# Kernel optimization log

Hardware: AMD Instinct MI355X
Metric: run time of the kernel (lower is better)

Reference implementation:

```python
import jax, jax.numpy as jnp
import numpy as np

TOPK = 2

def setup_inputs() -> dict:
    key = jax.random.key(0)
    ks = jax.random.split(key, 5)
    B, S, D, H, E = 2, 4096, 1024, 2048, 8
    x = jax.random.normal(ks[0], (B, S, D), dtype=jnp.float32)
    router_w = jax.random.normal(ks[1], (E, D), dtype=jnp.float32) * 0.02
    w1 = jax.random.normal(ks[2], (E, D, H), dtype=jnp.float32) * 0.02
    w3 = jax.random.normal(ks[3], (E, D, H), dtype=jnp.float32) * 0.02
    w2 = jax.random.normal(ks[4], (E, H, D), dtype=jnp.float32) * 0.02
    return {"x": x, "router_w": router_w, "w1": w1, "w3": w3, "w2": w2}

def reference(x, router_w, w1, w3, w2):
    B, S, D = x.shape
    E = router_w.shape[0]
    xf = x.reshape(-1, D)                      # [T, D]
    T = xf.shape[0]
    logits = (xf @ router_w.T).astype(jnp.float32)      # [T, E]
    weights, indices = jax.lax.top_k(logits, TOPK)      # [T, k]
    weights = jax.nn.softmax(weights, axis=-1).astype(x.dtype)
    prob = jax.nn.softmax(logits, axis=-1)              # [T, E] fp32
    P = prob.mean(axis=0).astype(x.dtype)               # [E]
    mask = jnp.zeros((T, E), jnp.float32).at[jnp.arange(T)[:, None], indices].set(1.0)
    f = mask.mean(axis=0).astype(x.dtype)               # [E]
    aux_loss = E * jnp.sum(f * P)
    out = jnp.zeros_like(xf)
    for e in range(E):
        # combine weight for expert e per token (0 if not routed here)
        coef = jnp.sum(jnp.where(indices == e, weights, jnp.zeros_like(weights)), axis=-1)  # [T]
        h = jax.nn.silu(xf @ w1[e]) * (xf @ w3[e])      # [T, H] SwiGLU
        out = out + coef[:, None] * (h @ w2[e])         # masked combine == gather/scatter
    return out.reshape(B, S, D), aux_loss
```

## Files before the change

kernel.cpp:

```cpp
#include <hip/hip_runtime.h>
#include <hip/hip_bf16.h>

#define TT 8192
#define DD 1024
#define HH 2048
#define EE 8

typedef __bf16 bf16x8 __attribute__((ext_vector_type(8)));
typedef float floatx4 __attribute__((ext_vector_type(4)));
typedef short shortx8 __attribute__((ext_vector_type(8)));

__device__ __forceinline__ short f2bf(float f) {
  unsigned u = __float_as_uint(f);
  u += 0x7fffu + ((u >> 16) & 1u);
  return (short)(u >> 16);
}

__device__ __forceinline__ float bf2f(short s) {
  return __uint_as_float(((unsigned)(unsigned short)s) << 16);
}

__device__ __forceinline__ void gld16(const void* g, void* l) {
  __builtin_amdgcn_global_load_lds((const __attribute__((address_space(1))) void*)g,
                                   (__attribute__((address_space(3))) void*)l, 16, 0, 0);
}

__global__ __launch_bounds__(256) void router_kernel(
    const float* __restrict__ x, const float* __restrict__ rw,
    int* __restrict__ cpad, float* __restrict__ ppad,
    int* __restrict__ list_token, float* __restrict__ list_coef,
    int* __restrict__ tokpk, float* __restrict__ tokcf,
    short* __restrict__ xb)
{
  __shared__ int   sE0[32], sE1[32], lcnt[EE], sbase[EE], lp0[32], lp1[32];
  __shared__ float sG0[32], sG1[32], sP[EE];
  const int tid = threadIdx.x;
  if (tid < EE) { sP[tid] = 0.f; lcnt[tid] = 0; }
  __syncthreads();
  const int lane = tid & 63, wv = tid >> 6;
  const int t0 = blockIdx.x * 32;
  for (int ti = 0; ti < 8; ++ti) {
    const int s = wv * 8 + ti;
    const int t = t0 + s;
    float sc[EE];
#pragma unroll
    for (int e = 0; e < EE; ++e) sc[e] = 0.f;
#pragma unroll
    for (int j = 0; j < 4; ++j) {
      float4 xv = *(const float4*)(x + (size_t)t * DD + j * 256 + lane * 4);
#pragma unroll
      for (int e = 0; e < EE; ++e) {
        float4 rv = *(const float4*)(rw + e * DD + j * 256 + lane * 4);
        sc[e] += xv.x * rv.x + xv.y * rv.y + xv.z * rv.z + xv.w * rv.w;
      }
      if (xb) {
        short4 sv = make_short4(f2bf(xv.x), f2bf(xv.y), f2bf(xv.z), f2bf(xv.w));
        *(short4*)(xb + (size_t)t * DD + j * 256 + lane * 4) = sv;
      }
    }
#pragma unroll
    for (int off = 32; off > 0; off >>= 1)
#pragma unroll
      for (int e = 0; e < EE; ++e)
        sc[e] += __shfl_down(sc[e], off);
    if (lane == 0) {
      int i0 = 0; float l0 = sc[0];
      for (int e = 1; e < EE; ++e) if (sc[e] > l0) { l0 = sc[e]; i0 = e; }
      int i1 = -1; float l1 = -3.4e38f;
      for (int e = 0; e < EE; ++e) if (e != i0 && sc[e] > l1) { l1 = sc[e]; i1 = e; }
      const float g0 = 1.f / (1.f + __expf(l1 - l0));
      float pr[EE]; float sum = 0.f;
      for (int e = 0; e < EE; ++e) { pr[e] = __expf(sc[e] - l0); sum += pr[e]; }
      const float inv = 1.f / sum;
      for (int e = 0; e < EE; ++e) atomicAdd(&sP[e], pr[e] * inv);
      sE0[s] = i0; sE1[s] = i1; sG0[s] = g0; sG1[s] = 1.f - g0;
    }
  }
  __syncthreads();
  if (tid < 32) {
    lp0[tid] = atomicAdd(&lcnt[sE0[tid]], 1);
    lp1[tid] = atomicAdd(&lcnt[sE1[tid]], 1);
  }
  __syncthreads();
  if (tid < EE) {
    sbase[tid] = atomicAdd(&cpad[tid * 16], lcnt[tid]);
    atomicAdd(&ppad[tid * 16], sP[tid]);
  }
  __syncthreads();
  if (tid < 32) {
    int e0 = sE0[tid], e1 = sE1[tid], t = t0 + tid;
    int p0 = sbase[e0] + lp0[tid];
    int p1 = sbase[e1] + lp1[tid];
    list_token[e0 * TT + p0] = t; list_coef[e0 * TT + p0] = sG0[tid];
    list_token[e1 * TT + p1] = t; list_coef[e1 * TT + p1] = sG1[tid];
    tokpk[t * 2]     = (e0 << 13) | p0;  tokcf[t * 2]     = sG0[tid];
    tokpk[t * 2 + 1] = (e1 << 13) | p1;  tokcf[t * 2 + 1] = sG1[tid];
  }
}

__global__ void aux_kernel(const int* __restrict__ cpad, const float* __restrict__ ppad,
                           int* __restrict__ offsets, float* __restrict__ out_aux)
{
  if (threadIdx.x == 0) {
    float aux = 0.f; int off = 0;
    for (int e = 0; e < EE; ++e) {
      aux += ((float)cpad[e * 16] / (float)TT) * (ppad[e * 16] / (float)TT);
      offsets[e] = off; off += cpad[e * 16];
    }
    *out_aux = aux * (float)EE;
  }
}

__global__ __launch_bounds__(256) void convt13_kernel(const float* __restrict__ w1,
                                                      const float* __restrict__ w3,
                                                      short* __restrict__ out)
{
  __shared__ short T[64 * 74];
  const int t = threadIdx.x;
  const int z = blockIdx.z;
  const int is3 = (z >= EE) ? 1 : 0;
  const int e = is3 ? (z - EE) : z;
  const float* in = (is3 ? w3 : w1) + (size_t)e * DD * HH;
  short* o = out + (size_t)e * DD * HH * 2;
  const int c0 = blockIdx.x * 64, r0 = blockIdx.y * 64;
#pragma unroll
  for (int p = 0; p < 4; ++p) {
    int r = p * 16 + (t >> 4), c4 = (t & 15) * 4;
    float4 v = *(const float4*)(in + (size_t)(r0 + r) * HH + c0 + c4);
    short4 s = make_short4(f2bf(v.x), f2bf(v.y), f2bf(v.z), f2bf(v.w));
    *(short4*)&T[r * 74 + c4] = s;
  }
  __syncthreads();
#pragma unroll
  for (int q = 0; q < 2; ++q) {
    int u = q * 256 + t;
    int oc = u >> 3, k8 = (u & 7) * 8;
    shortx8 s;
#pragma unroll
    for (int j = 0; j < 8; ++j) s[j] = T[(k8 + j) * 74 + oc];
    int c = c0 + oc;
    int grow = 2 * (c & ~31) + (c & 31) + (is3 ? 32 : 0);
    *(shortx8*)&o[(size_t)grow * DD + r0 + k8] = s;
  }
}

__global__ __launch_bounds__(256) void convt_kernel(const float* __restrict__ in, short* __restrict__ out,
                                                    int R, int C)
{
  __shared__ short T[64 * 74];
  const int t = threadIdx.x;
  in  += (size_t)blockIdx.z * R * C;
  out += (size_t)blockIdx.z * R * C;
  const int c0 = blockIdx.x * 64, r0 = blockIdx.y * 64;
#pragma unroll
  for (int p = 0; p < 4; ++p) {
    int r = p * 16 + (t >> 4), c4 = (t & 15) * 4;
    float4 v = *(const float4*)(in + (size_t)(r0 + r) * C + c0 + c4);
    short4 s = make_short4(f2bf(v.x), f2bf(v.y), f2bf(v.z), f2bf(v.w));
    *(short4*)&T[r * 74 + c4] = s;
  }
  __syncthreads();
#pragma unroll
  for (int q = 0; q < 2; ++q) {
    int u = q * 256 + t;
    int oc = u >> 3, k8 = (u & 7) * 8;
    shortx8 s;
#pragma unroll
    for (int j = 0; j < 8; ++j) s[j] = T[(k8 + j) * 74 + oc];
    *(shortx8*)&out[(size_t)(c0 + oc) * R + r0 + k8] = s;
  }
}


#define PH_BAR()  { __builtin_amdgcn_s_barrier(); __builtin_amdgcn_sched_barrier(0); }
#define WAITL0()  { asm volatile("s_waitcnt lgkmcnt(0)" ::: "memory"); __builtin_amdgcn_sched_barrier(0); }
#define WAITVN(n) { asm volatile("s_waitcnt vmcnt(" #n ")" ::: "memory"); __builtin_amdgcn_sched_barrier(0); }

template<int NT>
__device__ __forceinline__ void mma_core(char* SM, int tid,
    const char* a00, const char* a01, const char* a10, const char* a11,
    const char* b00, const char* b01, const char* b10, const char* b11,
    floatx4 (&acc)[8][4])
{
  const int lane = tid & 63, w = tid >> 6;
  const int l16 = lane & 15, quad = lane >> 4;
  const int wm = (w >> 2) & 1, wn = w & 3;
  const int cx = (((l16 >> 1) & 1) << 4) | (((l16 >> 2) & 1) << 5) | ((l16 & 1) << 6);
  const int ck0 = (quad * 16) ^ cx;
  const int arb = (wm * 128 + l16) * 128;
  const int brb = 32768 + (wn * 64 + l16) * 128;
  const int wq = w * 2048;

#define SA_(u,h,p0,p1) { gld16((p0) + (size_t)(u) * 128, SM + (((u) & 1) << 16) + (h) * 16384 + wq); \
                         gld16((p1) + (size_t)(u) * 128, SM + (((u) & 1) << 16) + (h) * 16384 + wq + 1024); }
#define SB_(u,h,p0,p1) { gld16((p0) + (size_t)(u) * 128, SM + (((u) & 1) << 16) + 32768 + (h) * 16384 + wq); \
                         gld16((p1) + (size_t)(u) * 128, SM + (((u) & 1) << 16) + 32768 + (h) * 16384 + wq + 1024); }
#define LA_(mi) { a[mi][0] = *(const bf16x8*)(SM + cur + arb + (mi) * 2048 + ck0); \
                  a[mi][1] = *(const bf16x8*)(SM + cur + arb + (mi) * 2048 + (ck0 ^ 64)); }
#define LB_(ni) { b[ni][0] = *(const bf16x8*)(SM + cur + brb + (ni) * 2048 + ck0); \
                  b[ni][1] = *(const bf16x8*)(SM + cur + brb + (ni) * 2048 + (ck0 ^ 64)); }
#define MM_(mi,ni) { acc[mi][ni] = __builtin_amdgcn_mfma_f32_16x16x32_bf16(a[mi][0], b[ni][0], acc[mi][ni], 0, 0, 0); \
                     acc[mi][ni] = __builtin_amdgcn_mfma_f32_16x16x32_bf16(a[mi][1], b[ni][1], acc[mi][ni], 0, 0, 0); }

  SA_(0, 0, a00, a01); SA_(0, 1, a10, a11);
  SB_(0, 0, b00, b01); SB_(0, 1, b10, b11);
  SA_(1, 0, a00, a01); SA_(1, 1, a10, a11);
  WAITVN(4);
  __builtin_amdgcn_s_barrier();
  __builtin_amdgcn_sched_barrier(0);

#pragma unroll 2
  for (int t = 0; t < NT; ++t) {
    const int cur = (t & 1) << 16;
    bf16x8 a[8][2], b[4][2];
    LA_(0) LA_(1) LA_(2) LA_(3) LB_(0) LB_(1)
    if (t + 1 < NT) SB_(t + 1, 0, b00, b01);
    PH_BAR(); WAITL0();
    __builtin_amdgcn_s_setprio(1);
    MM_(0,0) MM_(1,0) MM_(2,0) MM_(3,0) MM_(0,1) MM_(1,1) MM_(2,1) MM_(3,1)
    __builtin_amdgcn_s_setprio(0);
    PH_BAR();
    LA_(4) LA_(5) LA_(6) LA_(7) LB_(2) LB_(3)
    if (t + 1 < NT) SB_(t + 1, 1, b10, b11);
    PH_BAR(); WAITL0();
    __builtin_amdgcn_s_setprio(1);
    MM_(4,2) MM_(5,2) MM_(6,2) MM_(7,2) MM_(4,3) MM_(5,3) MM_(6,3) MM_(7,3)
    __builtin_amdgcn_s_setprio(0);
    PH_BAR();
    if (t + 2 < NT) SA_(t + 2, 0, a00, a01);
    PH_BAR();
    __builtin_amdgcn_s_setprio(1);
    MM_(0,2) MM_(1,2) MM_(2,2) MM_(3,2) MM_(0,3) MM_(1,3) MM_(2,3) MM_(3,3)
    __builtin_amdgcn_s_setprio(0);
    PH_BAR();
    if (t + 2 < NT) SA_(t + 2, 1, a10, a11);
    PH_BAR();
    __builtin_amdgcn_s_setprio(1);
    MM_(4,0) MM_(5,0) MM_(6,0) MM_(7,0) MM_(4,1) MM_(5,1) MM_(6,1) MM_(7,1)
    __builtin_amdgcn_s_setprio(0);
    if (t + 2 < NT) { WAITVN(4); } else { WAITVN(0); }
    PH_BAR();
  }
#undef SA_
#undef SB_
#undef LA_
#undef LB_
#undef MM_
}

__global__ __launch_bounds__(512, 2) void g1p_kernel(
    const short* __restrict__ xb, const short* __restrict__ w13t,
    const int* __restrict__ cpad, const int* __restrict__ offsets,
    const int* __restrict__ list_token, short* __restrict__ Hbuf)
{
  const int lin = blockIdx.x + 16 * (blockIdx.y + 32 * blockIdx.z);
  const int xcd = lin & 7, c = lin >> 3;
  const int e = c >> 6, rb = (c >> 1) & 31, nb = (xcd << 1) | (c & 1);
  const int cnt = cpad[e * 16];
  if (rb * 256 >= cnt) return;
  __shared__ char SM[131072];
  const int tid = threadIdx.x;
  const int lane = tid & 63, w = tid >> 6;
  const int srow = lane >> 3;
  const int scol = (((lane ^ (lane >> 4)) & 1) << 4)
                 | ((((lane >> 1) ^ (lane >> 5)) & 1) << 5)
                 | ((((lane >> 2) ^ (lane >> 3)) & 1) << 6);
  const int* lt = list_token + e * TT;
  const char* ap[2][2];
#pragma unroll
  for (int h = 0; h < 2; ++h)
#pragma unroll
    for (int i = 0; i < 2; ++i) {
      int gr = rb * 256 + h * 128 + (w * 2 + i) * 8 + srow;
      int tok = (gr < cnt) ? lt[gr] : lt[0];
      ap[h][i] = (const char*)xb + (size_t)tok * 2048 + scol;
    }
  const char* bb = (const char*)w13t + ((size_t)e * 4096 + nb * 256) * 2048
                 + (size_t)(w * 16 + srow) * 2048 + scol;
  floatx4 acc[8][4] = {};
  mma_core<16>(SM, tid, ap[0][0], ap[0][1], ap[1][0], ap[1][1],
               bb, bb + 8 * 2048, bb + 128 * 2048, bb + 136 * 2048, acc);
  const int off = offsets[e];
  const int l16 = lane & 15, quad = lane >> 4;
  const int wm = (w >> 2) & 1, wn = w & 3;
#pragma unroll
  for (int mi = 0; mi < 8; ++mi)
#pragma unroll
    for (int r = 0; r < 4; ++r) {
      int grow = rb * 256 + wm * 128 + mi * 16 + quad * 4 + r;
      if (grow < cnt) {
        size_t rowbase = (size_t)(off + grow) * HH + nb * 128 + wn * 32;
#pragma unroll
        for (int ni = 0; ni < 2; ++ni) {
          float aa = acc[mi][ni][r], bbv = acc[mi][ni + 2][r];
          float hv = aa / (1.f + __expf(-aa)) * bbv;
          Hbuf[rowbase + ni * 16 + l16] = f2bf(hv);
        }
      }
    }
}

__global__ __launch_bounds__(256, 2) void g2o_kernel(
    const short* __restrict__ Hbuf, const short* __restrict__ w2t,
    const int* __restrict__ cpad, const int* __restrict__ offsets,
    short* __restrict__ Obuf)
{
  const int lin = blockIdx.x + 8 * (blockIdx.y + 64 * blockIdx.z);
  const int xcd = lin & 7, c = lin >> 3;
  const int nb = xcd, e = c >> 6, rb = c & 63;
  const int cnt = cpad[e * 16];
  if (rb * 128 >= cnt) return;
  __shared__ short Asm[128 * 32];
  __shared__ short Bsm[128 * 32];
  const int tid = threadIdx.x, lane = tid & 63, wv = tid >> 6;
  const int wm = (wv >> 1) * 64, wn = (wv & 1) * 64;
  const int quad = lane >> 4, l16 = lane & 15;
  floatx4 acc[4][4] = {{{0.f}}};
  const int off = offsets[e];
  const int qrow = wv * 32 + (lane >> 2);
  const int qcb = (lane & 3) * 16;
  const char* ag = (const char*)(Hbuf + (size_t)(off + rb * 128 + qrow) * HH) + qcb;
  const char* bg = (const char*)(w2t + (size_t)e * DD * HH + (size_t)(nb * 128 + qrow) * HH) + qcb;
  char* al = (char*)Asm + wv * 2048;
  char* bl = (char*)Bsm + wv * 2048;
  int aro[4], bro[4];
#pragma unroll
  for (int mi = 0; mi < 4; ++mi) aro[mi] = (wm + mi * 16 + l16) * 32 + quad * 8;
#pragma unroll
  for (int ni = 0; ni < 4; ++ni) bro[ni] = (wn + ni * 16 + l16) * 32 + quad * 8;

  for (int k0 = 0; k0 < HH; k0 += 32) {
    __syncthreads();
    gld16(ag + (size_t)k0 * 2, al);
    gld16(ag + (size_t)k0 * 2 + 16 * HH * 2, al + 1024);
    gld16(bg + (size_t)k0 * 2, bl);
    gld16(bg + (size_t)k0 * 2 + 16 * HH * 2, bl + 1024);
    __syncthreads();
    bf16x8 af[4], bf[4];
#pragma unroll
    for (int mi = 0; mi < 4; ++mi) af[mi] = *(const bf16x8*)&Asm[aro[mi]];
#pragma unroll
    for (int ni = 0; ni < 4; ++ni) bf[ni] = *(const bf16x8*)&Bsm[bro[ni]];
#pragma unroll
    for (int mi = 0; mi < 4; ++mi)
#pragma unroll
      for (int ni = 0; ni < 4; ++ni)
        acc[mi][ni] = __builtin_amdgcn_mfma_f32_16x16x32_bf16(af[mi], bf[ni], acc[mi][ni], 0, 0, 0);
  }
#pragma unroll
  for (int mi = 0; mi < 4; ++mi)
#pragma unroll
    for (int r = 0; r < 4; ++r) {
      int row = wm + mi * 16 + quad * 4 + r;
      int grow = rb * 128 + row;
      if (grow < cnt) {
        short* orow = Obuf + (size_t)(off + grow) * DD + nb * 128 + wn;
#pragma unroll
        for (int ni = 0; ni < 4; ++ni)
          orow[ni * 16 + l16] = f2bf(acc[mi][ni][r]);
      }
    }
}

__global__ __launch_bounds__(256) void combine_kernel(
    const short* __restrict__ Obuf, const int* __restrict__ offsets,
    const int* __restrict__ tokpk, const float* __restrict__ tokcf,
    float* __restrict__ out)
{
  const int tid = threadIdx.x, lane = tid & 63, wv = tid >> 6;
  const int t = blockIdx.x * 4 + wv;
  const int pk0 = tokpk[t * 2], pk1 = tokpk[t * 2 + 1];
  const float c0 = tokcf[t * 2], c1 = tokcf[t * 2 + 1];
  const size_t r0 = (size_t)(offsets[pk0 >> 13] + (pk0 & 8191)) * DD;
  const size_t r1 = (size_t)(offsets[pk1 >> 13] + (pk1 & 8191)) * DD;
  float* orow = out + (size_t)t * DD;
#pragma unroll
  for (int p = 0; p < 2; ++p) {
    int cidx = p * 512 + lane * 8;
    shortx8 a = *(const shortx8*)(Obuf + r0 + cidx);
    shortx8 b = *(const shortx8*)(Obuf + r1 + cidx);
    float v[8];
#pragma unroll
    for (int j = 0; j < 8; ++j) v[j] = c0 * bf2f(a[j]) + c1 * bf2f(b[j]);
    *(float4*)(orow + cidx)     = make_float4(v[0], v[1], v[2], v[3]);
    *(float4*)(orow + cidx + 4) = make_float4(v[4], v[5], v[6], v[7]);
  }
}

__global__ __launch_bounds__(256, 2) void g1s_kernel(
    const float* __restrict__ x, const float* __restrict__ w1, const float* __restrict__ w3,
    const int* __restrict__ cpad, const int* __restrict__ offsets,
    const int* __restrict__ list_token, short* __restrict__ Hbuf)
{
  const int e = blockIdx.z, rb = blockIdx.y, nb = blockIdx.x;
  const int cnt = cpad[e * 16];
  if (rb * 128 >= cnt) return;
  __shared__ short Asm[128 * 40];
  __shared__ short B1sm[128 * 40];
  __shared__ short B3sm[128 * 40];
  const int tid = threadIdx.x, lane = tid & 63, wv = tid >> 6;
  const int wm = (wv >> 1) * 64, wn = (wv & 1) * 64;
  const int quad = lane >> 4, l16 = lane & 15;
  floatx4 acc1[4][4] = {{{0.f}}};
  floatx4 acc3[4][4] = {{{0.f}}};
  const int ar = tid >> 3, ak = (tid & 7) * 4;
  const int bp = tid & 63, bq = tid >> 6;
  const int bswz = (bq ^ ((bp >> 2) & 3)) * 8;
  const int bo0 = (2 * bp) * 40 + bswz, bo1 = bo0 + 40;
  int aro[4], bro[4];
#pragma unroll
  for (int mi = 0; mi < 4; ++mi) aro[mi] = (wm + mi * 16 + l16) * 40 + quad * 8;
#pragma unroll
  for (int ni = 0; ni < 4; ++ni) {
    int nl = wn + ni * 16 + l16;
    bro[ni] = nl * 40 + ((quad ^ ((nl >> 3) & 3)) * 8);
  }
  int tok[4];
#pragma unroll
  for (int i = 0; i < 4; ++i) {
    int gr = rb * 128 + ar + 32 * i;
    tok[i] = (gr < cnt) ? list_token[e * TT + gr] : list_token[e * TT];
  }
  const float* w1e = w1 + (size_t)e * DD * HH + (size_t)nb * 128;
  const float* w3e = w3 + (size_t)e * DD * HH + (size_t)nb * 128;
  for (int k0 = 0; k0 < DD; k0 += 32) {
    __syncthreads();
#pragma unroll
    for (int i = 0; i < 4; ++i) {
      int r = ar + 32 * i;
      float4 v = *(const float4*)(x + (size_t)tok[i] * DD + k0 + ak);
      short4 sv = make_short4(f2bf(v.x), f2bf(v.y), f2bf(v.z), f2bf(v.w));
      *(short4*)&Asm[r * 40 + ak] = sv;
    }
    {
      float2 u[8];
#pragma unroll
      for (int j = 0; j < 8; ++j) u[j] = *(const float2*)(w1e + (size_t)(k0 + bq * 8 + j) * HH + 2 * bp);
      shortx8 p0, p1;
#pragma unroll
      for (int j = 0; j < 8; ++j) { p0[j] = f2bf(u[j].x); p1[j] = f2bf(u[j].y); }
      *(shortx8*)&B1sm[bo0] = p0; *(shortx8*)&B1sm[bo1] = p1;
    }
    {
      float2 u[8];
#pragma unroll
      for (int j = 0; j < 8; ++j) u[j] = *(const float2*)(w3e + (size_t)(k0 + bq * 8 + j) * HH + 2 * bp);
      shortx8 p0, p1;
#pragma unroll
      for (int j = 0; j < 8; ++j) { p0[j] = f2bf(u[j].x); p1[j] = f2bf(u[j].y); }
      *(shortx8*)&B3sm[bo0] = p0; *(shortx8*)&B3sm[bo1] = p1;
    }
    __syncthreads();
    bf16x8 af[4], b1f[4], b3f[4];
#pragma unroll
    for (int mi = 0; mi < 4; ++mi) af[mi] = *(const bf16x8*)&Asm[aro[mi]];
#pragma unroll
    for (int ni = 0; ni < 4; ++ni) {
      b1f[ni] = *(const bf16x8*)&B1sm[bro[ni]];
      b3f[ni] = *(const bf16x8*)&B3sm[bro[ni]];
    }
#pragma unroll
    for (int mi = 0; mi < 4; ++mi)
#pragma unroll
      for (int ni = 0; ni < 4; ++ni) {
        acc1[mi][ni] = __builtin_amdgcn_mfma_f32_16x16x32_bf16(af[mi], b1f[ni], acc1[mi][ni], 0, 0, 0);
        acc3[mi][ni] = __builtin_amdgcn_mfma_f32_16x16x32_bf16(af[mi], b3f[ni], acc3[mi][ni], 0, 0, 0);
      }
  }
  const int off = offsets[e];
#pragma unroll
  for (int mi = 0; mi < 4; ++mi)
#pragma unroll
    for (int r = 0; r < 4; ++r) {
      int row = wm + mi * 16 + quad * 4 + r;
      int grow = rb * 128 + row;
      if (grow < cnt) {
        size_t rowbase = (size_t)(off + grow) * HH + (size_t)nb * 128 + wn;
#pragma unroll
        for (int ni = 0; ni < 4; ++ni) {
          float a = acc1[mi][ni][r], b = acc3[mi][ni][r];
          float h = a / (1.f + __expf(-a)) * b;
          Hbuf[rowbase + ni * 16 + l16] = f2bf(h);
        }
      }
    }
}

__global__ __launch_bounds__(256, 2) void g2s_kernel(
    const short* __restrict__ Hbuf, const float* __restrict__ w2,
    const int* __restrict__ cpad, const int* __restrict__ offsets,
    const int* __restrict__ list_token, const float* __restrict__ list_coef,
    float* __restrict__ out)
{
  const int e = blockIdx.z, rb = blockIdx.y, nb = blockIdx.x;
  const int cnt = cpad[e * 16];
  if (rb * 128 >= cnt) return;
  __shared__ short Asm[128 * 40];
  __shared__ short Bsm[128 * 40];
  const int tid = threadIdx.x, lane = tid & 63, wv = tid >> 6;
  const int wm = (wv >> 1) * 64, wn = (wv & 1) * 64;
  const int quad = lane >> 4, l16 = lane & 15;
  floatx4 acc[4][4] = {{{0.f}}};
  const int ar = tid >> 3, ak = (tid & 7) * 4;
  const int bp = tid & 63, bq = tid >> 6;
  const int bswz = (bq ^ ((bp >> 2) & 3)) * 8;
  const int bo0 = (2 * bp) * 40 + bswz, bo1 = bo0 + 40;
  int aro[4], bro[4];
#pragma unroll
  for (int mi = 0; mi < 4; ++mi) aro[mi] = (wm + mi * 16 + l16) * 40 + quad * 8;
#pragma unroll
  for (int ni = 0; ni < 4; ++ni) {
    int nl = wn + ni * 16 + l16;
    bro[ni] = nl * 40 + ((quad ^ ((nl >> 3) & 3)) * 8);
  }
  const int off = offsets[e];
  size_t hrow[4];
#pragma unroll
  for (int i = 0; i < 4; ++i) {
    int gr = rb * 128 + ar + 32 * i;
    int cg = (gr < cnt) ? gr : (cnt - 1);
    hrow[i] = (size_t)(off + cg) * HH;
  }
  const float* w2e = w2 + (size_t)e * HH * DD + (size_t)nb * 128;
  for (int k0 = 0; k0 < HH; k0 += 32) {
    __syncthreads();
#pragma unroll
    for (int i = 0; i < 4; ++i) {
      int r = ar + 32 * i;
      short4 sv = *(const short4*)(Hbuf + hrow[i] + k0 + ak);
      *(short4*)&Asm[r * 40 + ak] = sv;
    }
    {
      float2 u[8];
#pragma unroll
      for (int j = 0; j < 8; ++j) u[j] = *(const float2*)(w2e + (size_t)(k0 + bq * 8 + j) * DD + 2 * bp);
      shortx8 p0, p1;
#pragma unroll
      for (int j = 0; j < 8; ++j) { p0[j] = f2bf(u[j].x); p1[j] = f2bf(u[j].y); }
      *(shortx8*)&Bsm[bo0] = p0; *(shortx8*)&Bsm[bo1] = p1;
    }
    __syncthreads();
    bf16x8 af[4], bf[4];
#pragma unroll
    for (int mi = 0; mi < 4; ++mi) af[mi] = *(const bf16x8*)&Asm[aro[mi]];
#pragma unroll
    for (int ni = 0; ni < 4; ++ni) bf[ni] = *(const bf16x8*)&Bsm[bro[ni]];
#pragma unroll
    for (int mi = 0; mi < 4; ++mi)
#pragma unroll
      for (int ni = 0; ni < 4; ++ni)
        acc[mi][ni] = __builtin_amdgcn_mfma_f32_16x16x32_bf16(af[mi], bf[ni], acc[mi][ni], 0, 0, 0);
  }
#pragma unroll
  for (int mi = 0; mi < 4; ++mi)
#pragma unroll
    for (int r = 0; r < 4; ++r) {
      int row = wm + mi * 16 + quad * 4 + r;
      int grow = rb * 128 + row;
      if (grow < cnt) {
        int tokid = list_token[e * TT + grow];
        float coef = list_coef[e * TT + grow];
        float* orow = out + (size_t)tokid * DD + (size_t)nb * 128 + wn;
#pragma unroll
        for (int ni = 0; ni < 4; ++ni)
          atomicAdd(&orow[ni * 16 + l16], coef * acc[mi][ni][r]);
      }
    }
}

extern "C" void kernel_launch(void* const* d_in, const int* in_sizes, int n_in,
                              void* d_out, int out_size, void* d_ws, size_t ws_size,
                              hipStream_t stream)
{
  const float* x  = (const float*)d_in[0];
  const float* rw = (const float*)d_in[1];
  const float* w1 = (const float*)d_in[2];
  const float* w3 = (const float*)d_in[3];
  const float* w2 = (const float*)d_in[4];
  float* out = (float*)d_out;

  char* ws = (char*)d_ws;
  int*   cpad      = (int*)(ws + 0);
  float* ppad      = (float*)(ws + 512);
  int*   offsets   = (int*)(ws + 1024);
  int*   list_tok  = (int*)(ws + 4096);
  float* list_coef = (float*)(ws + 4096 + EE * TT * 4);
  int*   tokpk     = (int*)(ws + 4096 + 2 * EE * TT * 4);
  float* tokcf     = (float*)(ws + 4096 + 2 * EE * TT * 4 + 2 * TT * 4);

  const size_t OFF_W1T = 1u << 20;
  const size_t OFF_W3T = OFF_W1T + ((size_t)EE * DD * HH * 2);
  const size_t OFF_XBF = OFF_W3T + ((size_t)EE * DD * HH * 2);
  const size_t OFF_HB  = OFF_XBF + ((size_t)TT * DD * 2);
  const size_t NEED    = OFF_HB + ((size_t)(2 * TT + 128) * HH * 2);

  hipMemsetAsync(ws, 0, 1024, stream);

  const bool fast = (ws_size >= NEED);
  short* XBF = fast ? (short*)(ws + OFF_XBF) : nullptr;

  router_kernel<<<256, 256, 0, stream>>>(x, rw, cpad, ppad, list_tok, list_coef, tokpk, tokcf, XBF);
  aux_kernel<<<1, 64, 0, stream>>>(cpad, ppad, offsets, out + (size_t)TT * DD);

  if (fast) {
    short* W13T = (short*)(ws + OFF_W1T);
    short* OB   = (short*)(ws + OFF_W1T);
    short* W2T  = (short*)(ws + OFF_W3T);
    short* HB   = (short*)(ws + OFF_HB);
    convt13_kernel<<<dim3(HH / 64, DD / 64, 2 * EE), 256, 0, stream>>>(w1, w3, W13T);
    g1p_kernel<<<dim3(16, 32, EE), 512, 0, stream>>>(XBF, W13T, cpad, offsets, list_tok, HB);
    convt_kernel<<<dim3(DD / 64, HH / 64, EE), 256, 0, stream>>>(w2, W2T, HH, DD);
    g2o_kernel<<<dim3(8, 64, EE), 256, 0, stream>>>(HB, W2T, cpad, offsets, OB);
    combine_kernel<<<TT / 4, 256, 0, stream>>>(OB, offsets, tokpk, tokcf, out);
  } else {
    hipMemsetAsync(d_out, 0, (size_t)TT * DD * sizeof(float), stream);
    short* HB = (short*)(ws + (1 << 20));
    g1s_kernel<<<dim3(HH / 128, TT / 128, EE), 256, 0, stream>>>(x, w1, w3, cpad, offsets, list_tok, HB);
    g2s_kernel<<<dim3(DD / 128, TT / 128, EE), 256, 0, stream>>>(HB, w2, cpad, offsets, list_tok, list_coef, out);
  }
}
```

Measured before the change: 587.2 us.

## Rewrite down-projection GEMM to 256x256 tiles using shared pipelined mma_core

```diff
diff --git a/kernel.cpp b/kernel.cpp
--- a/kernel.cpp
+++ b/kernel.cpp
@@ -300,61 +300,45 @@
     }
 }
 
-__global__ __launch_bounds__(256, 2) void g2o_kernel(
+__global__ __launch_bounds__(512, 2) void g2q_kernel(
     const short* __restrict__ Hbuf, const short* __restrict__ w2t,
     const int* __restrict__ cpad, const int* __restrict__ offsets,
     short* __restrict__ Obuf)
 {
-  const int lin = blockIdx.x + 8 * (blockIdx.y + 64 * blockIdx.z);
-  const int xcd = lin & 7, c = lin >> 3;
-  const int nb = xcd, e = c >> 6, rb = c & 63;
+  const int nb = blockIdx.x, rb = blockIdx.y, e = blockIdx.z;
   const int cnt = cpad[e * 16];
-  if (rb * 128 >= cnt) return;
-  __shared__ short Asm[128 * 32];
-  __shared__ short Bsm[128 * 32];
-  const int tid = threadIdx.x, lane = tid & 63, wv = tid >> 6;
-  const int wm = (wv >> 1) * 64, wn = (wv & 1) * 64;
-  const int quad = lane >> 4, l16 = lane & 15;
-  floatx4 acc[4][4] = {{{0.f}}};
+  if (rb * 256 >= cnt) return;
+  __shared__ char SM[131072];
+  const int tid = threadIdx.x;
+  const int lane = tid & 63, w = tid >> 6;
+  const int srow = lane >> 3;
+  const int scol = (((lane ^ (lane >> 4)) & 1) << 4)
+                 | ((((lane >> 1) ^ (lane >> 5)) & 1) << 5)
+                 | ((((lane >> 2) ^ (lane >> 3)) & 1) << 6);
   const int off = offsets[e];
-  const int qrow = wv * 32 + (lane >> 2);
-  const int qcb = (lane & 3) * 16;
-  const char* ag = (const char*)(Hbuf + (size_t)(off + rb * 128 + qrow) * HH) + qcb;
-  const char* bg = (const char*)(w2t + (size_t)e * DD * HH + (size_t)(nb * 128 + qrow) * HH) + qcb;
-  char* al = (char*)Asm + wv * 2048;
-  char* bl = (char*)Bsm + wv * 2048;
-  int aro[4], bro[4];
-#pragma unroll
-  for (int mi = 0; mi < 4; ++mi) aro[mi] = (wm + mi * 16 + l16) * 32 + quad * 8;
-#pragma unroll
-  for (int ni = 0; ni < 4; ++ni) bro[ni] = (wn + ni * 16 + l16) * 32 + quad * 8;
-
-  for (int k0 = 0; k0 < HH; k0 += 32) {
-    __syncthreads();
-    gld16(ag + (size_t)k0 * 2, al);
-    gld16(ag + (size_t)k0 * 2 + 16 * HH * 2, al + 1024);
-    gld16(bg + (size_t)k0 * 2, bl);
-    gld16(bg + (size_t)k0 * 2 + 16 * HH * 2, bl + 1024);
-    __syncthreads();
-    bf16x8 af[4], bf[4];
-#pragma unroll
-    for (int mi = 0; mi < 4; ++mi) af[mi] = *(const bf16x8*)&Asm[aro[mi]];
-#pragma unroll
-    for (int ni = 0; ni < 4; ++ni) bf[ni] = *(const bf16x8*)&Bsm[bro[ni]];
-#pragma unroll
-    for (int mi = 0; mi < 4; ++mi)
-#pragma unroll
-      for (int ni = 0; ni < 4; ++ni)
-        acc[mi][ni] = __builtin_amdgcn_mfma_f32_16x16x32_bf16(af[mi], bf[ni], acc[mi][ni], 0, 0, 0);
-  }
-#pragma unroll
-  for (int mi = 0; mi < 4; ++mi)
+  const char* ap[2][2];
+#pragma unroll
+  for (int h = 0; h < 2; ++h)
+#pragma unroll
+    for (int i = 0; i < 2; ++i) {
+      int gr = rb * 256 + h * 128 + (w * 2 + i) * 8 + srow;
+      int cg = (gr < cnt) ? gr : (cnt - 1);
+      ap[h][i] = (const char*)Hbuf + (size_t)(off + cg) * 4096 + scol;
+    }
+  const char* bb = (const char*)w2t + ((size_t)e * DD + nb * 256) * 4096
+                 + (size_t)(w * 16 + srow) * 4096 + scol;
+  floatx4 acc[8][4] = {};
+  mma_core<32>(SM, tid, ap[0][0], ap[0][1], ap[1][0], ap[1][1],
+               bb, bb + 8 * 4096, bb + 128 * 4096, bb + 136 * 4096, acc);
+  const int l16 = lane & 15, quad = lane >> 4;
+  const int wm = (w >> 2) & 1, wn = w & 3;
+#pragma unroll
+  for (int mi = 0; mi < 8; ++mi)
 #pragma unroll
     for (int r = 0; r < 4; ++r) {
-      int row = wm + mi * 16 + quad * 4 + r;
-      int grow = rb * 128 + row;
+      int grow = rb * 256 + wm * 128 + mi * 16 + quad * 4 + r;
       if (grow < cnt) {
-        short* orow = Obuf + (size_t)(off + grow) * DD + nb * 128 + wn;
+        short* orow = Obuf + (size_t)(off + grow) * DD + nb * 256 + wn * 64;
 #pragma unroll
         for (int ni = 0; ni < 4; ++ni)
           orow[ni * 16 + l16] = f2bf(acc[mi][ni][r]);
@@ -610,7 +594,7 @@
     convt13_kernel<<<dim3(HH / 64, DD / 64, 2 * EE), 256, 0, stream>>>(w1, w3, W13T);
     g1p_kernel<<<dim3(16, 32, EE), 512, 0, stream>>>(XBF, W13T, cpad, offsets, list_tok, HB);
     convt_kernel<<<dim3(DD / 64, HH / 64, EE), 256, 0, stream>>>(w2, W2T, HH, DD);
-    g2o_kernel<<<dim3(8, 64, EE), 256, 0, stream>>>(HB, W2T, cpad, offsets, OB);
+    g2q_kernel<<<dim3(DD / 256, 32, EE), 512, 0, stream>>>(HB, W2T, cpad, offsets, OB);
     combine_kernel<<<TT / 4, 256, 0, stream>>>(OB, offsets, tokpk, tokcf, out);
   } else {
     hipMemsetAsync(d_out, 0, (size_t)TT * DD * sizeof(float), stream);
```

Result: no change. 592.4 us (+0.9%).
